# Kernel tuning notes

Hardware: AMD Instinct MI355X
Metric: run time of the kernel (lower is better)

## Reference

```python
import jax, jax.numpy as jnp
import numpy as np

D_MODEL = 1024
N_HEADS = 16
HEAD_DIM = D_MODEL // N_HEADS


def setup_inputs() -> dict:
    key = jax.random.key(0)
    ks = jax.random.split(key, 11)
    B, S = 4, 2048
    scale = 1.0 / np.sqrt(D_MODEL)
    inp = {
        "query": jax.random.normal(ks[0], (B, S, D_MODEL), jnp.float32),
        "key": jax.random.normal(ks[1], (B, S, D_MODEL), jnp.float32),
        "value": jax.random.normal(ks[2], (B, S, D_MODEL), jnp.float32),
        "Wq": jax.random.normal(ks[3], (D_MODEL, D_MODEL), jnp.float32) * scale,
        "bq": jnp.zeros((D_MODEL,), jnp.float32),
        "Wk": jax.random.normal(ks[4], (D_MODEL, D_MODEL), jnp.float32) * scale,
        "bk": jnp.zeros((D_MODEL,), jnp.float32),
        "Wv": jax.random.normal(ks[5], (D_MODEL, D_MODEL), jnp.float32) * scale,
        "bv": jnp.zeros((D_MODEL,), jnp.float32),
        "Wo": jax.random.normal(ks[6], (D_MODEL, D_MODEL), jnp.float32) * scale,
        "bo": jnp.zeros((D_MODEL,), jnp.float32),
    }
    return inp


def reference(query, key, value, Wq, bq, Wk, bk, Wv, bv, Wo, bo):
    B, S, _ = query.shape
    # QKV projections (nn.Linear: x @ W.T + b; weights here stored as [out,in])
    q = query @ Wq.T + bq
    k = key @ Wk.T + bk
    v = value @ Wv.T + bv
    # [B, S, H, Dh] -> [B, H, S, Dh]
    q = q.reshape(B, S, N_HEADS, HEAD_DIM).transpose(0, 2, 1, 3)
    k = k.reshape(B, S, N_HEADS, HEAD_DIM).transpose(0, 2, 1, 3)
    v = v.reshape(B, S, N_HEADS, HEAD_DIM).transpose(0, 2, 1, 3)
    # full score matrix [B, H, S, S]
    scores = jnp.einsum("bhqd,bhkd->bhqk", q, k) / jnp.sqrt(
        jnp.asarray(HEAD_DIM, q.dtype)
    )
    attn = jax.nn.softmax(scores, axis=-1)
    out = jnp.einsum("bhqk,bhkd->bhqd", attn, v)  # [B, H, S, Dh]
    out = out.transpose(0, 2, 1, 3).reshape(B, S, D_MODEL)
    return out @ Wo.T + bo
```

## Files before the change

kernel.cpp:

```cpp
#include <hip/hip_runtime.h>
#include <cstdint>
#include <cstddef>


typedef _Float16 h16;
typedef _Float16 h16x4 __attribute__((ext_vector_type(4)));
typedef _Float16 h16x8 __attribute__((ext_vector_type(8)));
typedef __fp16 fp16x2v __attribute__((ext_vector_type(2)));
typedef float f32x4 __attribute__((ext_vector_type(4)));
typedef float f32x16 __attribute__((ext_vector_type(16)));

#define SEQ 2048
#define HDIM 64

__device__ __forceinline__ void gld16(const void* g, void* l) {
  __builtin_amdgcn_global_load_lds((__attribute__((address_space(1))) void*)g,
                                   (__attribute__((address_space(3))) void*)l,
                                   16, 0, 0);
}

#define VMCNT_(n) asm volatile("s_waitcnt vmcnt(" #n ")" ::: "memory")
#define VMCNT(n) VMCNT_(n)

__device__ __forceinline__ void pl32swap(unsigned& a, unsigned& b) {
  asm volatile("v_permlane32_swap_b32 %0, %1" : "+v"(a), "+v"(b));
}

struct CvtArgs {
  const float* src[7];
  h16* dst[7];
  int n4[7];
};

__global__ __launch_bounds__(256) void cvt_kernel(CvtArgs a) {
  const int tk = blockIdx.y;
  const int n4 = a.n4[tk];
  const float4* s = (const float4*)a.src[tk];
  h16x4* d = (h16x4*)a.dst[tk];
  const int stride = gridDim.x * blockDim.x;
  for (int i = blockIdx.x * blockDim.x + threadIdx.x; i < n4; i += stride) {
    float4 v = s[i];
    h16x4 o = {(h16)v.x, (h16)v.y, (h16)v.z, (h16)v.w};
    d[i] = o;
  }
}

enum { EPI_Q = 0, EPI_V = 1, EPI_OUT = 2, EPI_K = 3 };

struct GemmArgs {
  const h16* A[3];
  const h16* W[3];
  const float* bias[3];
  void* dst[3];
  float scale[3];
  int epi[3];
};

__global__ __launch_bounds__(256) void gemm_h16(GemmArgs g) {
  __shared__ __align__(16) h16 sA[2][4096];
  __shared__ __align__(16) h16 sW[2][4096];

  const int lin =
      blockIdx.x + gridDim.x * (blockIdx.y + gridDim.y * blockIdx.z);
  const int total = gridDim.x * gridDim.y * gridDim.z;
  const int nid = (lin & 7) * (total >> 3) + (lin >> 3);
  const int per = gridDim.x * gridDim.y;
  const int z = nid / per;
  const int r = nid % per;
  const int n0 = (r % gridDim.x) * 128;
  const int m0 = (r / gridDim.x) * 128;

  const h16* A = g.A[z];
  const h16* W = g.W[z];
  const float* bias = g.bias[z];
  void* dst = g.dst[z];
  const float scale = g.scale[z];
  const int epi = g.epi[z];

  const int t = threadIdx.x;
  const int lane = t & 63, wave = t >> 6;
  const int lq = lane & 15, quad = lane >> 4;
  const int wm = wave & 1, wn = wave >> 1;

  const int bsl = lane >> 2;
  const int srcRow = (bsl & 14) | ((bsl ^ (bsl >> 2)) & 1);
  const int srcK = (lane & 3) ^ (srcRow & 3);
  const h16* AgS = A + (size_t)(m0 + wave * 32 + srcRow) * 1024 + srcK * 8;
  const h16* WgS = W + (size_t)(n0 + wave * 32 + srcRow) * 1024 + srcK * 8;

  const int rsw = (lq & 14) | ((lq ^ (lq >> 2)) & 1);
  const int aoff = rsw * 32 + (quad ^ (lq & 3)) * 8;

  f32x4 zero4 = {0.f, 0.f, 0.f, 0.f};
  f32x4 acc[4][4];
#pragma unroll
  for (int i = 0; i < 4; ++i)
#pragma unroll
    for (int j = 0; j < 4; ++j) acc[i][j] = zero4;

#define GSTAGE(SLOT, K0)                                                      \
  {                                                                           \
    gld16(AgS + (K0), &sA[SLOT][wave * 1024]);                                \
    gld16(AgS + (K0) + 16 * 1024, &sA[SLOT][wave * 1024 + 512]);              \
    gld16(WgS + (K0), &sW[SLOT][wave * 1024]);                                \
    gld16(WgS + (K0) + 16 * 1024, &sW[SLOT][wave * 1024 + 512]);              \
  }

#define GCOMP(SLOT)                                                           \
  {                                                                           \
    h16x8 af[4], wf[4];                                                       \
    _Pragma("unroll") for (int mt = 0; mt < 4; ++mt) {                        \
      af[mt] = *(const h16x8*)&sA[SLOT][(wm * 4 + mt) * 512 + aoff];          \
    }                                                                         \
    _Pragma("unroll") for (int nt = 0; nt < 4; ++nt) {                        \
      wf[nt] = *(const h16x8*)&sW[SLOT][(wn * 4 + nt) * 512 + aoff];          \
    }                                                                         \
    __builtin_amdgcn_s_setprio(1);                                            \
    _Pragma("unroll") for (int mt = 0; mt < 4; ++mt) {                        \
      _Pragma("unroll") for (int nt = 0; nt < 4; ++nt) {                      \
        acc[mt][nt] = __builtin_amdgcn_mfma_f32_16x16x32_f16(                 \
            af[mt], wf[nt], acc[mt][nt], 0, 0, 0);                            \
      }                                                                       \
    }                                                                         \
    __builtin_amdgcn_s_setprio(0);                                            \
  }

  GSTAGE(0, 0);
  GSTAGE(1, 32);

#pragma unroll 1
  for (int ti = 0; ti < 31; ++ti) {
    VMCNT(4);
    __builtin_amdgcn_s_barrier();
    __builtin_amdgcn_sched_barrier(0);
    const int slot = ti & 1;
    GCOMP(slot);
    __builtin_amdgcn_sched_barrier(0);
    __builtin_amdgcn_s_barrier();
    if (ti < 30) GSTAGE(slot, (ti + 2) * 32);
  }
  VMCNT(0);
  __builtin_amdgcn_s_barrier();
  __builtin_amdgcn_sched_barrier(0);
  GCOMP(1);

#undef GSTAGE
#undef GCOMP

  const int gmb = m0 + wm * 64;
  const int gnb = n0 + wn * 64;
#pragma unroll
  for (int mt = 0; mt < 4; ++mt) {
#pragma unroll
    for (int nt = 0; nt < 4; ++nt) {
      const int gn = gnb + nt * 16 + lq;
      const float bv = bias[gn];
#pragma unroll
      for (int rr = 0; rr < 4; ++rr) {
        const int gm = gmb + mt * 16 + quad * 4 + rr;
        const float v = (acc[mt][nt][rr] + bv) * scale;
        if (epi == EPI_OUT) {
          ((float*)dst)[(size_t)gm * 1024 + gn] = v;
        } else if (epi == EPI_Q) {
          const int b = gm >> 11, s = gm & 2047, h = gn >> 6, d = gn & 63;
          ((h16*)dst)[((size_t)(b * 16 + h) * 2048 + s) * 64 + d] = (h16)v;
        } else if (epi == EPI_K) {
          const int b = gm >> 11, s = gm & 2047, h = gn >> 6, d = gn & 63;
          const int dsw = (((d >> 3) ^ (s & 7)) << 3) | (d & 7);
          ((h16*)dst)[((size_t)(b * 16 + h) * 2048 + s) * 64 + dsw] = (h16)v;
        } else {
          const int b = gm >> 11, s = gm & 2047, h = gn >> 6, d = gn & 63;
          const int ssw =
              (s & ~127) | (((((s >> 3) & 15) ^ (d & 15))) << 3) | (s & 7);
          ((h16*)dst)[((size_t)(b * 16 + h) * 64 + d) * 2048 + ssw] = (h16)v;
        }
      }
    }
  }
}

__global__ __launch_bounds__(512, 2) void flash_fwd(
    const h16* __restrict__ Qp, const h16* __restrict__ Kp,
    const h16* __restrict__ Vtp, h16* __restrict__ attn) {
  __shared__ __align__(16) h16 sK[2][8192];
  __shared__ __align__(16) h16 sVt[2][8192];

  const int t = threadIdx.x, lane = t & 63, wave = t >> 6;
  const int l31 = lane & 31;
  const int h = lane >> 5;

  const int lin = blockIdx.x + (blockIdx.y << 3);
  const int nid = (lin & 7) * 64 + (lin >> 3);
  const int bh = nid >> 3, q0 = (nid & 7) * 256;

  const h16* Qh = Qp + (size_t)bh * SEQ * HDIM;
  const h16* Kh = Kp + (size_t)bh * SEQ * HDIM;
  const h16* Vh = Vtp + (size_t)bh * HDIM * SEQ;

  const int qrow = q0 + wave * 32 + l31;
  h16x8 bq[4];
#pragma unroll
  for (int ks = 0; ks < 4; ++ks)
    bq[ks] = *(const h16x8*)(Qh + (size_t)qrow * 64 + ks * 16 + h * 8);
  VMCNT(0);
  __builtin_amdgcn_sched_barrier(0);

  const int vr = lane >> 4;
  const int vc = (lane & 15) * 8;

  int colK[4], colV[8];
#pragma unroll
  for (int ks = 0; ks < 4; ++ks) colK[ks] = ((ks * 2 + h) ^ (l31 & 7)) * 8;
#pragma unroll
  for (int ks = 0; ks < 8; ++ks) colV[ks] = ((ks * 2 + h) ^ (l31 & 15)) * 8;

#define STAGE(SLOT, KT)                                                       \
  {                                                                           \
    const h16* gK = Kh + (size_t)(KT) * 64;                                   \
    gld16(gK + wave * 512 + lane * 8, &sK[SLOT][wave * 512]);                 \
    gld16(gK + (wave + 8) * 512 + lane * 8, &sK[SLOT][(wave + 8) * 512]);     \
    gld16(Vh + (size_t)(4 * wave + vr) * SEQ + (KT) + vc,                     \
          &sVt[SLOT][wave * 512]);                                            \
    gld16(Vh + (size_t)(4 * (wave + 8) + vr) * SEQ + (KT) + vc,               \
          &sVt[SLOT][(wave + 8) * 512]);                                      \
  }

  f32x16 zero16 = {};
  f32x16 oT[2];
  oT[0] = zero16;
  oT[1] = zero16;
  float lsum = 0.f;

#define COMPUTE(SLOT)                                                         \
  {                                                                           \
    _Pragma("unroll") for (int mt = 0; mt < 4; ++mt) {                        \
      f32x16 s = zero16;                                                      \
      __builtin_amdgcn_s_setprio(1);                                          \
      _Pragma("unroll") for (int ks = 0; ks < 4; ++ks) {                      \
        h16x8 ak =                                                            \
            *(const h16x8*)&sK[SLOT][(mt * 32 + l31) * 64 + colK[ks]];        \
        s = __builtin_amdgcn_mfma_f32_32x32x16_f16(ak, bq[ks], s, 0, 0, 0);   \
      }                                                                       \
      __builtin_amdgcn_s_setprio(0);                                          \
      uint2 pk[4];                                                            \
      _Pragma("unroll") for (int g = 0; g < 4; ++g) {                         \
        const float e0 = __builtin_amdgcn_exp2f(s[g * 4 + 0]);                \
        const float e1 = __builtin_amdgcn_exp2f(s[g * 4 + 1]);                \
        const float e2 = __builtin_amdgcn_exp2f(s[g * 4 + 2]);                \
        const float e3 = __builtin_amdgcn_exp2f(s[g * 4 + 3]);                \
        lsum += (e0 + e1) + (e2 + e3);                                        \
        fp16x2v c0 = __builtin_amdgcn_cvt_pkrtz(e0, e1);                      \
        fp16x2v c1 = __builtin_amdgcn_cvt_pkrtz(e2, e3);                      \
        pk[g].x = __builtin_bit_cast(unsigned, c0);                           \
        pk[g].y = __builtin_bit_cast(unsigned, c1);                           \
      }                                                                       \
      _Pragma("unroll") for (int ks2 = 0; ks2 < 2; ++ks2) {                   \
        const int ks = mt * 2 + ks2;                                          \
        unsigned ax = pk[2 * ks2].x, ay = pk[2 * ks2].y;                      \
        unsigned bx = pk[2 * ks2 + 1].x, by = pk[2 * ks2 + 1].y;              \
        pl32swap(ax, bx);                                                     \
        pl32swap(ay, by);                                                     \
        uint4 bp32 = {ax, ay, bx, by};                                        \
        h16x8 bp = __builtin_bit_cast(h16x8, bp32);                           \
        __builtin_amdgcn_s_setprio(1);                                        \
        _Pragma("unroll") for (int dt = 0; dt < 2; ++dt) {                    \
          h16x8 av =                                                          \
              *(const h16x8*)&sVt[SLOT][(dt * 32 + l31) * 128 + colV[ks]];    \
          oT[dt] = __builtin_amdgcn_mfma_f32_32x32x16_f16(av, bp, oT[dt], 0,  \
                                                          0, 0);              \
        }                                                                     \
        __builtin_amdgcn_s_setprio(0);                                       \
      }                                                                       \
    }                                                                         \
  }

  STAGE(0, 0);
  STAGE(1, 128);

#pragma unroll 1
  for (int ti = 0; ti < 15; ++ti) {
    VMCNT(4);
    __builtin_amdgcn_s_barrier();
    __builtin_amdgcn_sched_barrier(0);
    const int slot = ti & 1;
    COMPUTE(slot);
    __builtin_amdgcn_sched_barrier(0);
    __builtin_amdgcn_s_barrier();
    if (ti < 14) STAGE(slot, (ti + 2) * 128);
  }
  VMCNT(0);
  __builtin_amdgcn_s_barrier();
  __builtin_amdgcn_sched_barrier(0);
  COMPUTE(1);

#undef STAGE
#undef COMPUTE

  lsum += __shfl_xor(lsum, 32);
  const float inv = 1.f / lsum;

  const int b = bh >> 4, head = bh & 15;
  h16* orow = attn + ((size_t)(b * SEQ + qrow)) * 1024 + head * 64;
#pragma unroll
  for (int dt = 0; dt < 2; ++dt) {
#pragma unroll
    for (int g = 0; g < 4; ++g) {
      h16x4 ov = {(h16)(oT[dt][g * 4 + 0] * inv), (h16)(oT[dt][g * 4 + 1] * inv),
                  (h16)(oT[dt][g * 4 + 2] * inv), (h16)(oT[dt][g * 4 + 3] * inv)};
      *(h16x4*)&orow[dt * 32 + g * 8 + h * 4] = ov;
    }
  }
}

extern "C" void kernel_launch(void* const* d_in, const int* in_sizes, int n_in,
                              void* d_out, int out_size, void* d_ws,
                              size_t ws_size, hipStream_t stream) {
  (void)in_sizes; (void)n_in; (void)out_size;

  const float* query = (const float*)d_in[0];
  const float* key   = (const float*)d_in[1];
  const float* value = (const float*)d_in[2];
  const float* Wq = (const float*)d_in[3];
  const float* bq = (const float*)d_in[4];
  const float* Wk = (const float*)d_in[5];
  const float* bk = (const float*)d_in[6];
  const float* Wv = (const float*)d_in[7];
  const float* bv = (const float*)d_in[8];
  const float* Wo = (const float*)d_in[9];
  const float* bo = (const float*)d_in[10];

  char* ws = (char*)d_ws;
  const size_t MB = 1024 * 1024;
  h16* xq = (h16*)(ws);
  h16* xk = (h16*)(ws + 16 * MB);
  h16* xv = (h16*)(ws + 32 * MB);
  h16* qperm = (h16*)(ws + 48 * MB);
  h16 *kperm, *vperm, *attn, *w16;
  const bool fused = ws_size >= 104 * MB;
  if (fused) {
    kperm = (h16*)(ws + 64 * MB);
    vperm = (h16*)(ws + 80 * MB);
    w16   = (h16*)(ws + 96 * MB);
    attn  = (h16*)(ws);
  } else {
    kperm = (h16*)(ws);
    vperm = (h16*)(ws + 16 * MB);
    attn  = (h16*)(ws + 32 * MB);
    w16   = (h16*)(ws + 64 * MB);
  }
  h16* wq16 = w16;
  h16* wk16 = w16 + 1048576;
  h16* wv16 = w16 + 2 * 1048576;
  h16* wo16 = w16 + 3 * 1048576;

  CvtArgs ca;
  const float* csrc[7] = {query, key, value, Wq, Wk, Wv, Wo};
  h16* cdst[7] = {xq, xk, xv, wq16, wk16, wv16, wo16};
  const int cn4[7] = {2097152, 2097152, 2097152, 262144, 262144, 262144, 262144};
  for (int i = 0; i < 7; ++i) { ca.src[i] = csrc[i]; ca.dst[i] = cdst[i]; ca.n4[i] = cn4[i]; }
  cvt_kernel<<<dim3(512, 7), 256, 0, stream>>>(ca);

  const float qscale = 0.125f * 1.4426950408889634f;
  if (fused) {
    GemmArgs ga;
    ga.A[0] = xq; ga.A[1] = xk; ga.A[2] = xv;
    ga.W[0] = wq16; ga.W[1] = wk16; ga.W[2] = wv16;
    ga.bias[0] = bq; ga.bias[1] = bk; ga.bias[2] = bv;
    ga.dst[0] = qperm; ga.dst[1] = kperm; ga.dst[2] = vperm;
    ga.scale[0] = qscale; ga.scale[1] = 1.f; ga.scale[2] = 1.f;
    ga.epi[0] = EPI_Q; ga.epi[1] = EPI_K; ga.epi[2] = EPI_V;
    gemm_h16<<<dim3(8, 64, 3), 256, 0, stream>>>(ga);
  } else {
    const h16* As[3] = {xq, xk, xv};
    const h16* Ws[3] = {wq16, wk16, wv16};
    const float* bs[3] = {bq, bk, bv};
    h16* ds[3] = {qperm, kperm, vperm};
    const float scl[3] = {qscale, 1.f, 1.f};
    const int ep[3] = {EPI_Q, EPI_K, EPI_V};
    for (int i = 0; i < 3; ++i) {
      GemmArgs ga;
      for (int j = 0; j < 3; ++j) {
        ga.A[j] = As[i]; ga.W[j] = Ws[i]; ga.bias[j] = bs[i];
        ga.dst[j] = ds[i]; ga.scale[j] = scl[i]; ga.epi[j] = ep[i];
      }
      gemm_h16<<<dim3(8, 64, 1), 256, 0, stream>>>(ga);
    }
  }

  flash_fwd<<<dim3(8, 64), 512, 0, stream>>>(qperm, kperm, vperm, attn);

  GemmArgs go;
  for (int j = 0; j < 3; ++j) {
    go.A[j] = attn; go.W[j] = wo16; go.bias[j] = bo;
    go.dst[j] = d_out; go.scale[j] = 1.f; go.epi[j] = EPI_OUT;
  }
  gemm_h16<<<dim3(8, 64, 1), 256, 0, stream>>>(go);
}
```

Baseline: 377.2 us.

## Add 256x256-tile, 512-thread GEMM kernel for QKV projections

Adds a new gemm256 kernel that computes 256x256 output tiles with 8 waves, each wave owning a 128x64 sub-tile. The fused and unfused QKV projection launches switch to it, while the output projection keeps the old 128x128 kernel. The larger tiles cut global and L2 traffic per FLOP and double the accumulator work per wave. In exchange, the new kernel drops the XOR-swizzled LDS layout, which risks LDS bank conflicts, raises register pressure, and launches fewer blocks (384 instead of 1536).

```diff
diff --git a/kernel.cpp b/kernel.cpp
--- a/kernel.cpp
+++ b/kernel.cpp
@@ -56,9 +56,29 @@
   int epi[3];
 };
 
-__global__ __launch_bounds__(256) void gemm_h16(GemmArgs g) {
-  __shared__ __align__(16) h16 sA[2][4096];
-  __shared__ __align__(16) h16 sW[2][4096];
+__device__ __forceinline__ void epi_store(void* dst, int epi, float scale,
+                                          const float* bias, int gm, int gn,
+                                          float accv) {
+  const float v = (accv + bias[gn]) * scale;
+  if (epi == EPI_OUT) {
+    ((float*)dst)[(size_t)gm * 1024 + gn] = v;
+  } else if (epi == EPI_Q) {
+    const int b = gm >> 11, s = gm & 2047, h = gn >> 6, d = gn & 63;
+    ((h16*)dst)[((size_t)(b * 16 + h) * 2048 + s) * 64 + d] = (h16)v;
+  } else if (epi == EPI_K) {
+    const int b = gm >> 11, s = gm & 2047, h = gn >> 6, d = gn & 63;
+    const int dsw = (((d >> 3) ^ (s & 7)) << 3) | (d & 7);
+    ((h16*)dst)[((size_t)(b * 16 + h) * 2048 + s) * 64 + dsw] = (h16)v;
+  } else {
+    const int b = gm >> 11, s = gm & 2047, h = gn >> 6, d = gn & 63;
+    const int ssw = (s & ~127) | (((((s >> 3) & 15) ^ (d & 15))) << 3) | (s & 7);
+    ((h16*)dst)[((size_t)(b * 16 + h) * 64 + d) * 2048 + ssw] = (h16)v;
+  }
+}
+
+__global__ __launch_bounds__(512, 2) void gemm256(GemmArgs g) {
+  __shared__ __align__(16) h16 sA[2][8192];
+  __shared__ __align__(16) h16 sW[2][8192];
 
   const int lin =
       blockIdx.x + gridDim.x * (blockIdx.y + gridDim.y * blockIdx.z);
@@ -67,8 +87,8 @@
   const int per = gridDim.x * gridDim.y;
   const int z = nid / per;
   const int r = nid % per;
-  const int n0 = (r % gridDim.x) * 128;
-  const int m0 = (r / gridDim.x) * 128;
+  const int n0 = (r % gridDim.x) * 256;
+  const int m0 = (r / gridDim.x) * 256;
 
   const h16* A = g.A[z];
   const h16* W = g.W[z];
@@ -80,43 +100,43 @@
   const int t = threadIdx.x;
   const int lane = t & 63, wave = t >> 6;
   const int lq = lane & 15, quad = lane >> 4;
-  const int wm = wave & 1, wn = wave >> 1;
-
-  const int bsl = lane >> 2;
-  const int srcRow = (bsl & 14) | ((bsl ^ (bsl >> 2)) & 1);
-  const int srcK = (lane & 3) ^ (srcRow & 3);
-  const h16* AgS = A + (size_t)(m0 + wave * 32 + srcRow) * 1024 + srcK * 8;
-  const h16* WgS = W + (size_t)(n0 + wave * 32 + srcRow) * 1024 + srcK * 8;
-
-  const int rsw = (lq & 14) | ((lq ^ (lq >> 2)) & 1);
-  const int aoff = rsw * 32 + (quad ^ (lq & 3)) * 8;
+  const int wm = wave >> 2, wn = wave & 3;
+
+  const int srow = lane >> 2;
+  const int scol = (lane & 3) * 8;
+  const h16* Ag0 = A + (size_t)(m0 + wave * 16 + srow) * 1024 + scol;
+  const h16* Ag1 = A + (size_t)(m0 + 128 + wave * 16 + srow) * 1024 + scol;
+  const h16* Wg0 = W + (size_t)(n0 + wave * 16 + srow) * 1024 + scol;
+  const h16* Wg1 = W + (size_t)(n0 + 128 + wave * 16 + srow) * 1024 + scol;
 
   f32x4 zero4 = {0.f, 0.f, 0.f, 0.f};
-  f32x4 acc[4][4];
-#pragma unroll
-  for (int i = 0; i < 4; ++i)
+  f32x4 acc[8][4];
+#pragma unroll
+  for (int i = 0; i < 8; ++i)
 #pragma unroll
     for (int j = 0; j < 4; ++j) acc[i][j] = zero4;
 
 #define GSTAGE(SLOT, K0)                                                      \
   {                                                                           \
-    gld16(AgS + (K0), &sA[SLOT][wave * 1024]);                                \
-    gld16(AgS + (K0) + 16 * 1024, &sA[SLOT][wave * 1024 + 512]);              \
-    gld16(WgS + (K0), &sW[SLOT][wave * 1024]);                                \
-    gld16(WgS + (K0) + 16 * 1024, &sW[SLOT][wave * 1024 + 512]);              \
+    gld16(Ag0 + (K0), &sA[SLOT][wave * 512]);                                 \
+    gld16(Ag1 + (K0), &sA[SLOT][4096 + wave * 512]);                          \
+    gld16(Wg0 + (K0), &sW[SLOT][wave * 512]);                                 \
+    gld16(Wg1 + (K0), &sW[SLOT][4096 + wave * 512]);                          \
   }
 
 #define GCOMP(SLOT)                                                           \
   {                                                                           \
-    h16x8 af[4], wf[4];                                                       \
-    _Pragma("unroll") for (int mt = 0; mt < 4; ++mt) {                        \
-      af[mt] = *(const h16x8*)&sA[SLOT][(wm * 4 + mt) * 512 + aoff];          \
+    h16x8 af[8], wf[4];                                                       \
+    _Pragma("unroll") for (int mt = 0; mt < 8; ++mt) {                        \
+      af[mt] = *(const h16x8*)&sA[SLOT][(wm * 128 + mt * 16 + lq) * 32 +      \
+                                        quad * 8];                            \
     }                                                                         \
     _Pragma("unroll") for (int nt = 0; nt < 4; ++nt) {                        \
-      wf[nt] = *(const h16x8*)&sW[SLOT][(wn * 4 + nt) * 512 + aoff];          \
+      wf[nt] = *(const h16x8*)&sW[SLOT][(wn * 64 + nt * 16 + lq) * 32 +       \
+                                        quad * 8];                            \
     }                                                                         \
     __builtin_amdgcn_s_setprio(1);                                            \
-    _Pragma("unroll") for (int mt = 0; mt < 4; ++mt) {                        \
+    _Pragma("unroll") for (int mt = 0; mt < 8; ++mt) {                        \
       _Pragma("unroll") for (int nt = 0; nt < 4; ++nt) {                      \
         acc[mt][nt] = __builtin_amdgcn_mfma_f32_16x16x32_f16(                 \
             af[mt], wf[nt], acc[mt][nt], 0, 0, 0);                            \
@@ -147,6 +167,113 @@
 #undef GSTAGE
 #undef GCOMP
 
+  const int gmb = m0 + wm * 128;
+  const int gnb = n0 + wn * 64;
+#pragma unroll
+  for (int mt = 0; mt < 8; ++mt) {
+#pragma unroll
+    for (int nt = 0; nt < 4; ++nt) {
+      const int gn = gnb + nt * 16 + lq;
+#pragma unroll
+      for (int rr = 0; rr < 4; ++rr) {
+        const int gm = gmb + mt * 16 + quad * 4 + rr;
+        epi_store(dst, epi, scale, bias, gm, gn, acc[mt][nt][rr]);
+      }
+    }
+  }
+}
+
+__global__ __launch_bounds__(256) void gemm_h16(GemmArgs g) {
+  __shared__ __align__(16) h16 sA[2][4096];
+  __shared__ __align__(16) h16 sW[2][4096];
+
+  const int lin =
+      blockIdx.x + gridDim.x * (blockIdx.y + gridDim.y * blockIdx.z);
+  const int total = gridDim.x * gridDim.y * gridDim.z;
+  const int nid = (lin & 7) * (total >> 3) + (lin >> 3);
+  const int per = gridDim.x * gridDim.y;
+  const int z = nid / per;
+  const int r = nid % per;
+  const int n0 = (r % gridDim.x) * 128;
+  const int m0 = (r / gridDim.x) * 128;
+
+  const h16* A = g.A[z];
+  const h16* W = g.W[z];
+  const float* bias = g.bias[z];
+  void* dst = g.dst[z];
+  const float scale = g.scale[z];
+  const int epi = g.epi[z];
+
+  const int t = threadIdx.x;
+  const int lane = t & 63, wave = t >> 6;
+  const int lq = lane & 15, quad = lane >> 4;
+  const int wm = wave & 1, wn = wave >> 1;
+
+  const int bsl = lane >> 2;
+  const int srcRow = (bsl & 14) | ((bsl ^ (bsl >> 2)) & 1);
+  const int srcK = (lane & 3) ^ (srcRow & 3);
+  const h16* AgS = A + (size_t)(m0 + wave * 32 + srcRow) * 1024 + srcK * 8;
+  const h16* WgS = W + (size_t)(n0 + wave * 32 + srcRow) * 1024 + srcK * 8;
+
+  const int rsw = (lq & 14) | ((lq ^ (lq >> 2)) & 1);
+  const int aoff = rsw * 32 + (quad ^ (lq & 3)) * 8;
+
+  f32x4 zero4 = {0.f, 0.f, 0.f, 0.f};
+  f32x4 acc[4][4];
+#pragma unroll
+  for (int i = 0; i < 4; ++i)
+#pragma unroll
+    for (int j = 0; j < 4; ++j) acc[i][j] = zero4;
+
+#define GSTAGE(SLOT, K0)                                                      \
+  {                                                                           \
+    gld16(AgS + (K0), &sA[SLOT][wave * 1024]);                                \
+    gld16(AgS + (K0) + 16 * 1024, &sA[SLOT][wave * 1024 + 512]);              \
+    gld16(WgS + (K0), &sW[SLOT][wave * 1024]);                                \
+    gld16(WgS + (K0) + 16 * 1024, &sW[SLOT][wave * 1024 + 512]);              \
+  }
+
+#define GCOMP(SLOT)                                                           \
+  {                                                                           \
+    h16x8 af[4], wf[4];                                                       \
+    _Pragma("unroll") for (int mt = 0; mt < 4; ++mt) {                        \
+      af[mt] = *(const h16x8*)&sA[SLOT][(wm * 4 + mt) * 512 + aoff];          \
+    }                                                                         \
+    _Pragma("unroll") for (int nt = 0; nt < 4; ++nt) {                        \
+      wf[nt] = *(const h16x8*)&sW[SLOT][(wn * 4 + nt) * 512 + aoff];          \
+    }                                                                         \
+    __builtin_amdgcn_s_setprio(1);                                            \
+    _Pragma("unroll") for (int mt = 0; mt < 4; ++mt) {                        \
+      _Pragma("unroll") for (int nt = 0; nt < 4; ++nt) {                      \
+        acc[mt][nt] = __builtin_amdgcn_mfma_f32_16x16x32_f16(                 \
+            af[mt], wf[nt], acc[mt][nt], 0, 0, 0);                            \
+      }                                                                       \
+    }                                                                         \
+    __builtin_amdgcn_s_setprio(0);                                            \
+  }
+
+  GSTAGE(0, 0);
+  GSTAGE(1, 32);
+
+#pragma unroll 1
+  for (int ti = 0; ti < 31; ++ti) {
+    VMCNT(4);
+    __builtin_amdgcn_s_barrier();
+    __builtin_amdgcn_sched_barrier(0);
+    const int slot = ti & 1;
+    GCOMP(slot);
+    __builtin_amdgcn_sched_barrier(0);
+    __builtin_amdgcn_s_barrier();
+    if (ti < 30) GSTAGE(slot, (ti + 2) * 32);
+  }
+  VMCNT(0);
+  __builtin_amdgcn_s_barrier();
+  __builtin_amdgcn_sched_barrier(0);
+  GCOMP(1);
+
+#undef GSTAGE
+#undef GCOMP
+
   const int gmb = m0 + wm * 64;
   const int gnb = n0 + wn * 64;
 #pragma unroll
@@ -154,26 +281,10 @@
 #pragma unroll
     for (int nt = 0; nt < 4; ++nt) {
       const int gn = gnb + nt * 16 + lq;
-      const float bv = bias[gn];
 #pragma unroll
       for (int rr = 0; rr < 4; ++rr) {
         const int gm = gmb + mt * 16 + quad * 4 + rr;
-        const float v = (acc[mt][nt][rr] + bv) * scale;
-        if (epi == EPI_OUT) {
-          ((float*)dst)[(size_t)gm * 1024 + gn] = v;
-        } else if (epi == EPI_Q) {
-          const int b = gm >> 11, s = gm & 2047, h = gn >> 6, d = gn & 63;
-          ((h16*)dst)[((size_t)(b * 16 + h) * 2048 + s) * 64 + d] = (h16)v;
-        } else if (epi == EPI_K) {
-          const int b = gm >> 11, s = gm & 2047, h = gn >> 6, d = gn & 63;
-          const int dsw = (((d >> 3) ^ (s & 7)) << 3) | (d & 7);
-          ((h16*)dst)[((size_t)(b * 16 + h) * 2048 + s) * 64 + dsw] = (h16)v;
-        } else {
-          const int b = gm >> 11, s = gm & 2047, h = gn >> 6, d = gn & 63;
-          const int ssw =
-              (s & ~127) | (((((s >> 3) & 15) ^ (d & 15))) << 3) | (s & 7);
-          ((h16*)dst)[((size_t)(b * 16 + h) * 64 + d) * 2048 + ssw] = (h16)v;
-        }
+        epi_store(dst, epi, scale, bias, gm, gn, acc[mt][nt][rr]);
       }
     }
   }
@@ -369,7 +480,7 @@
     ga.dst[0] = qperm; ga.dst[1] = kperm; ga.dst[2] = vperm;
     ga.scale[0] = qscale; ga.scale[1] = 1.f; ga.scale[2] = 1.f;
     ga.epi[0] = EPI_Q; ga.epi[1] = EPI_K; ga.epi[2] = EPI_V;
-    gemm_h16<<<dim3(8, 64, 3), 256, 0, stream>>>(ga);
+    gemm256<<<dim3(4, 32, 3), 512, 0, stream>>>(ga);
   } else {
     const h16* As[3] = {xq, xk, xv};
     const h16* Ws[3] = {wq16, wk16, wv16};
@@ -383,7 +494,7 @@
         ga.A[j] = As[i]; ga.W[j] = Ws[i]; ga.bias[j] = bs[i];
         ga.dst[j] = ds[i]; ga.scale[j] = scl[i]; ga.epi[j] = ep[i];
       }
-      gemm_h16<<<dim3(8, 64, 1), 256, 0, stream>>>(ga);
+      gemm256<<<dim3(4, 32, 1), 512, 0, stream>>>(ga);
     }
   }
 
```

Measured after the change: 417.6 us. 1.11x slower.
